# Kernel optimization log

Hardware: AMD Instinct MI355X
Metric: run time of the kernel (lower is better)

Reference implementation:

```python
import jax, jax.numpy as jnp
import numpy as np

B, S, D, H, FF = 2, 2048, 1024, 16, 4096
HD = D // H
EPS = 1e-9


def setup_inputs() -> dict:
    key = jax.random.key(0)
    ks = jax.random.split(key, 16)
    sc = 0.02
    inp = {
        "x": jax.random.normal(ks[0], (B, S, D), jnp.float32),
        "y": jax.random.normal(ks[1], (B, S, D), jnp.float32),
        "decoder_mask": jnp.tril(jnp.ones((S, S), jnp.int32))[None, None],  # [1,1,S,S]
        # self-attention params (weights stored [in,out])
        "qkv_w": jax.random.normal(ks[2], (D, 3 * D), jnp.float32) * sc,
        "qkv_b": jnp.zeros((3 * D,), jnp.float32),
        "sa_fc_w": jax.random.normal(ks[3], (D, D), jnp.float32) * sc,
        "sa_fc_b": jnp.zeros((D,), jnp.float32),
        "g1": jnp.ones((D,), jnp.float32),
        "b1": jnp.zeros((D,), jnp.float32),
        # cross-attention params
        "kv_w": jax.random.normal(ks[4], (D, 2 * D), jnp.float32) * sc,
        "kv_b": jnp.zeros((2 * D,), jnp.float32),
        "q_w": jax.random.normal(ks[5], (D, D), jnp.float32) * sc,
        "q_b": jnp.zeros((D,), jnp.float32),
        "ca_fc_w": jax.random.normal(ks[6], (D, D), jnp.float32) * sc,
        "ca_fc_b": jnp.zeros((D,), jnp.float32),
        "g2": jnp.ones((D,), jnp.float32),
        "b2": jnp.zeros((D,), jnp.float32),
        # FFN params
        "ff1_w": jax.random.normal(ks[7], (D, FF), jnp.float32) * sc,
        "ff1_b": jnp.zeros((FF,), jnp.float32),
        "ff2_w": jax.random.normal(ks[8], (FF, D), jnp.float32) * sc,
        "ff2_b": jnp.zeros((D,), jnp.float32),
        "g3": jnp.ones((D,), jnp.float32),
        "b3": jnp.zeros((D,), jnp.float32),
    }
    return inp


def _layernorm(x, g, b):
    mean = jnp.mean(x, axis=-1, keepdims=True)
    var = jnp.mean((x - mean) ** 2, axis=-1, keepdims=True)
    return g * (x - mean) / jnp.sqrt(var + EPS) + b


def _sdpa(q, k, v, mask=None):
    # q,k,v: [B,H,S,hd]
    scores = jnp.einsum("bhqd,bhkd->bhqk", q, k) / jnp.sqrt(jnp.float32(q.shape[-1]))
    if mask is not None:
        scores = jnp.where(mask == 0, jnp.float32(-1e9), scores)
    attn = jax.nn.softmax(scores, axis=-1)
    return jnp.einsum("bhqk,bhkd->bhqd", attn, v)


def reference(x, y, decoder_mask, qkv_w, qkv_b, sa_fc_w, sa_fc_b, g1, b1,
              kv_w, kv_b, q_w, q_b, ca_fc_w, ca_fc_b, g2, b2,
              ff1_w, ff1_b, ff2_w, ff2_b, g3, b3):
    b, s, d = y.shape
    # --- masked self-attention on y ---
    qkv = (y @ qkv_w + qkv_b).reshape(b, s, H, 3 * HD).transpose(0, 2, 1, 3)
    q, k, v = jnp.split(qkv, 3, axis=-1)
    vals = _sdpa(q, k, v, decoder_mask).transpose(0, 2, 1, 3).reshape(b, s, d)
    sa = vals @ sa_fc_w + sa_fc_b
    y = _layernorm(sa + y, g1, b1)
    # --- cross-attention: kv from x, q from y ---
    kv = (x @ kv_w + kv_b).reshape(b, s, H, 2 * HD).transpose(0, 2, 1, 3)
    k2, v2 = jnp.split(kv, 2, axis=-1)
    q2 = (y @ q_w + q_b).reshape(b, s, H, HD).transpose(0, 2, 1, 3)
    vals2 = _sdpa(q2, k2, v2, None).transpose(0, 2, 1, 3).reshape(b, s, d)
    ca = vals2 @ ca_fc_w + ca_fc_b
    y = _layernorm(ca + y, g2, b2)
    # --- FFN ---
    h = jax.nn.relu(y @ ff1_w + ff1_b)
    ff = h @ ff2_w + ff2_b
    y = _layernorm(ff + y, g3, b3)
    return y
```

## Files before the change

kernel.cpp:

```cpp
#include <hip/hip_runtime.h>

typedef unsigned short u16;
typedef unsigned int u32;
typedef __attribute__((ext_vector_type(4))) float f32x4;
typedef __attribute__((ext_vector_type(8))) __bf16 bf16x8;
typedef __attribute__((ext_vector_type(2))) __bf16 bf16x2;
typedef __attribute__((ext_vector_type(4))) u16 u16x4;

#define NB 2
#define NS 2048
#define ND 1024
#define NH 16
#define NHD 64
#define NFF 4096
#define NBS (NB * NS)

typedef const __attribute__((address_space(1))) unsigned int as1_u32;
typedef __attribute__((address_space(3))) unsigned int as3_u32;

__device__ __forceinline__ void gl_lds16(const u16* g, u16* l) {
  __builtin_amdgcn_global_load_lds((as1_u32*)g, (as3_u32*)l, 16, 0, 0);
}

__device__ __forceinline__ u16 f2bf(float f) {
  union { float f; unsigned u; } v; v.f = f;
  unsigned r = (v.u + 0x7FFFu + ((v.u >> 16) & 1u)) >> 16;
  return (u16)r;
}

__device__ __forceinline__ float bf2f(u16 u) {
  union { u32 u; float f; } v; v.u = ((u32)u) << 16; return v.f;
}

__device__ __forceinline__ u32 pkbf(float a, float b) {
  bf16x2 v; v[0] = (__bf16)a; v[1] = (__bf16)b;
  union { bf16x2 v; u32 u; } c; c.v = v; return c.u;
}

__device__ __forceinline__ char* lswz(void* base, int row, int bcol) {
  return (char*)base + row * 128 + (bcol ^ ((row & 7) << 4));
}
__device__ __forceinline__ const char* lswz(const void* base, int row, int bcol) {
  return (const char*)base + row * 128 + (bcol ^ ((row & 7) << 4));
}

__global__ __launch_bounds__(256) void conv_bf16(const float* __restrict__ in,
                                                 u16* __restrict__ out, int n4) {
  int i = blockIdx.x * 256 + threadIdx.x;
  if (i >= n4) return;
  f32x4 v = *reinterpret_cast<const f32x4*>(&in[(size_t)i * 4]);
  u16x4 o;
#pragma unroll
  for (int j = 0; j < 4; ++j) o[j] = f2bf(v[j]);
  *reinterpret_cast<u16x4*>(&out[(size_t)i * 4]) = o;
}

struct WSeg { const float* src; u16* dst; int N; int tile0; };
struct WAll { WSeg s[7]; };

__global__ void wconv_all(WAll wa) {
  __shared__ float t[32][33];
  int bid = blockIdx.x;
  int si = 0;
#pragma unroll
  for (int i = 1; i < 7; ++i) si += (bid >= wa.s[i].tile0) ? 1 : 0;
  const WSeg sg = wa.s[si];
  const int tt = bid - sg.tile0;
  const int tilesx = sg.N >> 5;
  const int n0 = (tt % tilesx) * 32, k0 = (tt / tilesx) * 32;
  const int K = (si == 6) ? NFF : ND;
  int tx = threadIdx.x, ty = threadIdx.y;
#pragma unroll
  for (int i = ty; i < 32; i += 8) t[i][tx] = sg.src[(size_t)(k0 + i) * sg.N + n0 + tx];
  __syncthreads();
#pragma unroll
  for (int i = ty; i < 32; i += 8)
    sg.dst[(size_t)(n0 + i) * K + k0 + tx] = f2bf(t[tx][i]);
}

template <int TM, int OUTF32, int RELU>
__global__ __launch_bounds__(256) void gemm_bt(const u16* __restrict__ A,
                                               const u16* __restrict__ BT,
                                               const float* __restrict__ bias,
                                               float* __restrict__ Cf,
                                               u16* __restrict__ Cb,
                                               int M, int N, int K) {
  constexpr int MR = TM / 32;
  constexpr int ACH = TM / 64;
  __shared__ __align__(16) u16 lA[2][TM * 32];
  __shared__ __align__(16) u16 lB[2][128 * 32];
  const int tid = threadIdx.x;
  const int lane = tid & 63, wave = tid >> 6;
  const int bm = blockIdx.y * TM, bn = blockIdx.x * 128;
  const int wr = (wave >> 1) * (MR * 16), wc = (wave & 1) * 64;
  const int r16 = lane & 15, kg = lane >> 4;

  f32x4 acc[MR][4] = {};

  auto stage = [&](int buf, int k0) {
#pragma unroll
    for (int c = 0; c < ACH; ++c) {
      int chunk = c * 256 + tid;
      int r = chunk >> 2, kc = (chunk & 3) * 8;
      gl_lds16(&A[(size_t)(bm + r) * K + k0 + kc], &lA[buf][(c * 256 + wave * 64) * 8]);
    }
#pragma unroll
    for (int c = 0; c < 2; ++c) {
      int chunk = c * 256 + tid;
      int r = chunk >> 2, kc = (chunk & 3) * 8;
      gl_lds16(&BT[(size_t)(bn + r) * K + k0 + kc], &lB[buf][(c * 256 + wave * 64) * 8]);
    }
  };

  stage(0, 0);
  __syncthreads();

  const int nk = K / 32;
  for (int i = 0; i < nk; ++i) {
    const int cur = i & 1;
    if (i + 1 < nk) stage(cur ^ 1, (i + 1) * 32);

    bf16x8 af[MR], bfr[4];
#pragma unroll
    for (int m = 0; m < MR; ++m)
      af[m] = *reinterpret_cast<const bf16x8*>(&lA[cur][(wr + m * 16 + r16) * 32 + kg * 8]);
#pragma unroll
    for (int n = 0; n < 4; ++n)
      bfr[n] = *reinterpret_cast<const bf16x8*>(&lB[cur][(wc + n * 16 + r16) * 32 + kg * 8]);
#pragma unroll
    for (int m = 0; m < MR; ++m)
#pragma unroll
      for (int n = 0; n < 4; ++n)
        acc[m][n] = __builtin_amdgcn_mfma_f32_16x16x32_bf16(af[m], bfr[n], acc[m][n], 0, 0, 0);

    __syncthreads();
  }

#pragma unroll
  for (int m = 0; m < MR; ++m) {
    int row = bm + wr + m * 16 + kg * 4;
#pragma unroll
    for (int n = 0; n < 4; ++n) {
      int col = bn + wc + n * 16 + r16;
      float bv = bias[col];
#pragma unroll
      for (int j = 0; j < 4; ++j) {
        float v = acc[m][n][j] + bv;
        if (RELU) v = fmaxf(v, 0.f);
        if (OUTF32)
          Cf[(size_t)(row + j) * N + col] = v;
        else
          Cb[(size_t)(row + j) * N + col] = f2bf(v);
      }
    }
  }
}

__global__ __launch_bounds__(256) void vt_kern(const u16* __restrict__ src, int stride,
                                               int hmul, int hadd, u16* __restrict__ VT) {
  __shared__ u16 lt[64][72];
  const int bh = blockIdx.y;
  const int b = bh >> 4, h = bh & 15;
  const int s0 = blockIdx.x * 64;
  const u16* sb = src + (size_t)b * NS * stride + h * hmul + hadd;
#pragma unroll
  for (int c = 0; c < 2; ++c) {
    int chunk = c * 256 + threadIdx.x;
    int r = chunk >> 3, d = (chunk & 7) * 8;
    *reinterpret_cast<uint4*>(&lt[r][d]) =
        *reinterpret_cast<const uint4*>(&sb[(size_t)(s0 + r) * stride + d]);
  }
  __syncthreads();
  const int d = threadIdx.x >> 2, sq = (threadIdx.x & 3) * 16;
  union { u16 e[16]; uint4 v[2]; } pk;
#pragma unroll
  for (int i = 0; i < 16; ++i) pk.e[i] = lt[sq + i][d];
  uint4* dst = reinterpret_cast<uint4*>(&VT[((size_t)bh * NHD + d) * NS + s0 + sq]);
  dst[0] = pk.v[0];
  dst[1] = pk.v[1];
}

#define C1F 0.180336880f
#define OPSZ ((size_t)32 * NS * NHD)

template <int CAUSAL>
__global__ __launch_bounds__(512) void attn10(const u16* __restrict__ Qp, int qstride,
                                              int qhm, const u16* __restrict__ Kp,
                                              int kstride, int khm, int kha,
                                              const u16* __restrict__ VT,
                                              u16* __restrict__ OP,
                                              float2* __restrict__ ML) {
  const int bid = blockIdx.x;
  const int split = blockIdx.y;
  const int xcd = bid & 7, j5 = bid >> 3;
  const int bh = xcd + 8 * (j5 >> 3);
  int qt = j5 & 7;
  if (CAUSAL) qt = 7 - qt;
  const int b = bh >> 4, h = bh & 15;
  const int tid = threadIdx.x, lane = tid & 63, wave = tid >> 6;
  const int r16 = lane & 15, kg = lane >> 4;
  const int q0w = qt * 256 + wave * 32;

  __shared__ __align__(16) char lK[2][64 * 128];
  __shared__ __align__(16) char lV[2][64 * 128];
  __shared__ __align__(16) char lP[8][16 * 128];
  char* lPw = &lP[wave][0];

  const u16* qb = Qp + (size_t)b * NS * qstride + h * qhm;
  const u16* kb = Kp + (size_t)b * NS * kstride + h * khm + kha;
  const u16* vb = VT + (size_t)bh * NHD * NS;

  const int srow = tid >> 3;
  const int sbcol = (tid & 7) * 16;
  const int scol = (tid & 7) * 8;

  bf16x8 qf[2][2];
#pragma unroll
  for (int qn = 0; qn < 2; ++qn)
#pragma unroll
    for (int ks = 0; ks < 2; ++ks) {
      bf16x8 v = *reinterpret_cast<const bf16x8*>(
          &qb[(size_t)(q0w + qn * 16 + r16) * qstride + ks * 32 + kg * 8]);
#pragma unroll
      for (int e = 0; e < 8; ++e) v[e] = (__bf16)((float)v[e] * C1F);
      qf[qn][ks] = v;
    }

  f32x4 o_acc[2][4] = {};
  float m_run[2] = {-1e30f, -1e30f}, l_lane[2] = {0.f, 0.f};

  const int ntb = CAUSAL ? (4 * qt + 4) : (NS / 64);
  const int wnt = CAUSAL ? (q0w / 64 + 1) : (NS / 64);
  const int halfb = (ntb + 1) >> 1;
  const int t0 = split ? halfb : 0;
  const int t1 = split ? ntb : halfb;

  uint4 kreg, vreg;
  auto ldregs = [&](int t) {
    const int kv0 = t * 64;
    kreg = *reinterpret_cast<const uint4*>(&kb[(size_t)(kv0 + srow) * kstride + scol]);
    vreg = *reinterpret_cast<const uint4*>(&vb[(size_t)srow * NS + kv0 + scol]);
  };
  auto wrlds = [&](int buf) {
    *reinterpret_cast<uint4*>(lswz(lK[buf], srow, sbcol)) = kreg;
    *reinterpret_cast<uint4*>(lswz(lV[buf], srow, sbcol)) = vreg;
  };

  ldregs(t0);
  wrlds(0);
  __syncthreads();

  for (int t = t0; t < t1; ++t) {
    const int cur = (t - t0) & 1;
    const bool more = (t + 1 < t1);
    if (more) ldregs(t + 1);

    if (t < wnt) {
      const int kv0 = t * 64;
      const char* lKc = lK[cur];
      const char* lVc = lV[cur];

      bf16x8 kf[8];
#pragma unroll
      for (int c = 0; c < 4; ++c)
#pragma unroll
        for (int ks = 0; ks < 2; ++ks)
          kf[c * 2 + ks] = *reinterpret_cast<const bf16x8*>(
              lswz(lKc, c * 16 + r16, ks * 64 + kg * 16));

      f32x4 s[2][4] = {};
#pragma unroll
      for (int c = 0; c < 4; ++c)
#pragma unroll
        for (int ks = 0; ks < 2; ++ks) {
          s[0][c] = __builtin_amdgcn_mfma_f32_16x16x32_bf16(kf[c * 2 + ks], qf[0][ks], s[0][c], 0, 0, 0);
          s[1][c] = __builtin_amdgcn_mfma_f32_16x16x32_bf16(kf[c * 2 + ks], qf[1][ks], s[1][c], 0, 0, 0);
        }

      bf16x8 vf[8];
#pragma unroll
      for (int cd = 0; cd < 4; ++cd)
#pragma unroll
        for (int ks = 0; ks < 2; ++ks)
          vf[cd * 2 + ks] = *reinterpret_cast<const bf16x8*>(
              lswz(lVc, cd * 16 + r16, ks * 64 + kg * 16));

#pragma unroll
      for (int qn = 0; qn < 2; ++qn) {
        if (CAUSAL && t == wnt - 1) {
          const int q = q0w + qn * 16 + r16;
#pragma unroll
          for (int c = 0; c < 4; ++c)
#pragma unroll
            for (int j = 0; j < 4; ++j)
              if (kv0 + c * 16 + kg * 4 + j > q) s[qn][c][j] = -1e31f;
        }
        float m0 = fmaxf(fmaxf(s[qn][0][0], s[qn][0][1]), fmaxf(s[qn][0][2], s[qn][0][3]));
        float m1 = fmaxf(fmaxf(s[qn][1][0], s[qn][1][1]), fmaxf(s[qn][1][2], s[qn][1][3]));
        float m2 = fmaxf(fmaxf(s[qn][2][0], s[qn][2][1]), fmaxf(s[qn][2][2], s[qn][2][3]));
        float m3 = fmaxf(fmaxf(s[qn][3][0], s[qn][3][1]), fmaxf(s[qn][3][2], s[qn][3][3]));
        float mxr = fmaxf(fmaxf(m0, m1), fmaxf(m2, m3));
        float mn = m_run[qn];
        if (!__all(mxr <= mn + 8.f)) {
          float mz = mxr;
          mz = fmaxf(mz, __shfl_xor(mz, 16));
          mz = fmaxf(mz, __shfl_xor(mz, 32));
          mn = fmaxf(m_run[qn], mz);
          const float cr = exp2f(m_run[qn] - mn);
          m_run[qn] = mn;
          l_lane[qn] *= cr;
          float crow[4];
#pragma unroll
          for (int j = 0; j < 4; ++j) crow[j] = __shfl(cr, kg * 4 + j);
#pragma unroll
          for (int cd = 0; cd < 4; ++cd)
#pragma unroll
            for (int j = 0; j < 4; ++j) o_acc[qn][cd][j] *= crow[j];
        }
        float su = 0.f;
#pragma unroll
        for (int c = 0; c < 4; ++c)
#pragma unroll
          for (int j = 0; j < 4; ++j) {
            float p = exp2f(s[qn][c][j] - mn);
            s[qn][c][j] = p;
            su += p;
          }
        l_lane[qn] += su;

#pragma unroll
        for (int c = 0; c < 4; ++c) {
          uint2 w2 = {pkbf(s[qn][c][0], s[qn][c][1]), pkbf(s[qn][c][2], s[qn][c][3])};
          *reinterpret_cast<uint2*>(lswz(lPw, r16, c * 32 + kg * 8)) = w2;
        }
        bf16x8 pf[2];
#pragma unroll
        for (int ks = 0; ks < 2; ++ks)
          pf[ks] = *reinterpret_cast<const bf16x8*>(
              lswz(lPw, r16, ks * 64 + kg * 16));
#pragma unroll
        for (int cd = 0; cd < 4; ++cd)
#pragma unroll
          for (int ks = 0; ks < 2; ++ks)
            o_acc[qn][cd] = __builtin_amdgcn_mfma_f32_16x16x32_bf16(
                pf[ks], vf[cd * 2 + ks], o_acc[qn][cd], 0, 0, 0);
      }
    }

    if (more) wrlds(cur ^ 1);
    __syncthreads();
  }

  u16* op = OP + split * OPSZ + (size_t)bh * NS * NHD;
#pragma unroll
  for (int qn = 0; qn < 2; ++qn) {
    float l = l_lane[qn];
    l += __shfl_xor(l, 16);
    l += __shfl_xor(l, 32);
#pragma unroll
    for (int cd = 0; cd < 4; ++cd) {
      int col = cd * 16 + r16;
#pragma unroll
      for (int j = 0; j < 4; ++j) {
        int row = q0w + qn * 16 + kg * 4 + j;
        op[(size_t)row * NHD + col] = f2bf(o_acc[qn][cd][j]);
      }
    }
    if (kg == 0)
      ML[(size_t)split * 32 * NS + (size_t)bh * NS + q0w + qn * 16 + r16] =
          make_float2(m_run[qn], l);
  }
}

__global__ __launch_bounds__(256) void attn_comb(const u16* __restrict__ OP,
                                                 const float2* __restrict__ ML,
                                                 u16* __restrict__ AO) {
  int idx = blockIdx.x * 256 + threadIdx.x;
  int dg = (idx & 7) * 8;
  int q = (idx >> 3) & (NS - 1);
  int bh = idx >> 14;
  int b = bh >> 4, h = bh & 15;
  float2 ml0 = ML[(size_t)bh * NS + q];
  float2 ml1 = ML[(size_t)32 * NS + (size_t)bh * NS + q];
  float M = fmaxf(ml0.x, ml1.x);
  float w0 = exp2f(ml0.x - M), w1 = exp2f(ml1.x - M);
  float linv = 1.f / (ml0.y * w0 + ml1.y * w1);
  w0 *= linv;
  w1 *= linv;
  size_t src = ((size_t)bh * NS + q) * NHD + dg;
  uint4 r0 = *reinterpret_cast<const uint4*>(&OP[src]);
  uint4 r1 = *reinterpret_cast<const uint4*>(&OP[OPSZ + src]);
  const u16* e0 = reinterpret_cast<const u16*>(&r0);
  const u16* e1 = reinterpret_cast<const u16*>(&r1);
  u16 out[8];
#pragma unroll
  for (int j = 0; j < 8; ++j)
    out[j] = f2bf(bf2f(e0[j]) * w0 + bf2f(e1[j]) * w1);
  *reinterpret_cast<uint4*>(&AO[((size_t)b * NS + q) * ND + h * NHD + dg]) =
      *reinterpret_cast<uint4*>(out);
}

__global__ __launch_bounds__(256) void ln_kern(const float* __restrict__ a,
                                               const float* __restrict__ resid,
                                               const float* __restrict__ g,
                                               const float* __restrict__ bb,
                                               float* __restrict__ outf,
                                               u16* __restrict__ outb) {
  const int row = blockIdx.x;
  const int tid = threadIdx.x;
  const size_t off = (size_t)row * ND + tid * 4;
  f32x4 v = *reinterpret_cast<const f32x4*>(&a[off]);
  f32x4 r = *reinterpret_cast<const f32x4*>(&resid[off]);
#pragma unroll
  for (int j = 0; j < 4; ++j) v[j] += r[j];
  float s = v[0] + v[1] + v[2] + v[3];
  float s2 = v[0] * v[0] + v[1] * v[1] + v[2] * v[2] + v[3] * v[3];
#pragma unroll
  for (int m = 1; m < 64; m <<= 1) {
    s += __shfl_xor(s, m);
    s2 += __shfl_xor(s2, m);
  }
  __shared__ float ws1[4], ws2[4];
  int wave = tid >> 6, lane = tid & 63;
  if (lane == 0) { ws1[wave] = s; ws2[wave] = s2; }
  __syncthreads();
  s = ws1[0] + ws1[1] + ws1[2] + ws1[3];
  s2 = ws2[0] + ws2[1] + ws2[2] + ws2[3];
  float mean = s * (1.f / ND);
  float var = fmaxf(s2 * (1.f / ND) - mean * mean, 0.f);
  float rstd = rsqrtf(var + 1e-9f);
  f32x4 gg = *reinterpret_cast<const f32x4*>(&g[tid * 4]);
  f32x4 bv = *reinterpret_cast<const f32x4*>(&bb[tid * 4]);
  f32x4 o;
  u16x4 ob;
#pragma unroll
  for (int j = 0; j < 4; ++j) {
    o[j] = gg[j] * (v[j] - mean) * rstd + bv[j];
    ob[j] = f2bf(o[j]);
  }
  *reinterpret_cast<f32x4*>(&outf[off]) = o;
  *reinterpret_cast<u16x4*>(&outb[off]) = ob;
}

extern "C" void kernel_launch(void* const* d_in, const int* in_sizes, int n_in,
                              void* d_out, int out_size, void* d_ws, size_t ws_size,
                              hipStream_t stream) {
  const float* x = (const float*)d_in[0];
  const float* y = (const float*)d_in[1];
  const float* qkv_w = (const float*)d_in[3];
  const float* qkv_b = (const float*)d_in[4];
  const float* sa_fc_w = (const float*)d_in[5];
  const float* sa_fc_b = (const float*)d_in[6];
  const float* g1 = (const float*)d_in[7];
  const float* b1 = (const float*)d_in[8];
  const float* kv_w = (const float*)d_in[9];
  const float* kv_b = (const float*)d_in[10];
  const float* q_w = (const float*)d_in[11];
  const float* q_b = (const float*)d_in[12];
  const float* ca_fc_w = (const float*)d_in[13];
  const float* ca_fc_b = (const float*)d_in[14];
  const float* g2 = (const float*)d_in[15];
  const float* b2 = (const float*)d_in[16];
  const float* ff1_w = (const float*)d_in[17];
  const float* ff1_b = (const float*)d_in[18];
  const float* ff2_w = (const float*)d_in[19];
  const float* ff2_b = (const float*)d_in[20];
  const float* g3 = (const float*)d_in[21];
  const float* b3 = (const float*)d_in[22];

  if (ws_size < (120ull << 20)) return;

  char* w = (char*)d_ws;
  u16* Wqkv = (u16*)w;
  u16* Wsa  = Wqkv + 3145728;
  u16* Wkv  = Wsa + 1048576;
  u16* Wq   = Wkv + 2097152;
  u16* Wca  = Wq + 1048576;
  u16* Wff1 = Wca + 1048576;
  u16* Wff2 = Wff1 + 4194304;
  u16* ACT = (u16*)(w + (32ull << 20));
  u16* XB  = (u16*)(w + (40ull << 20));
  u16* Qb  = (u16*)(w + (48ull << 20));
  u16* VT  = (u16*)(w + (56ull << 20));
  u16* G   = (u16*)(w + (64ull << 20));
  float* Fa = (float*)(w + (88ull << 20));
  float* Fb = (float*)(w + (104ull << 20));
  u16* H   = XB;
  u16* AO  = G;
  u16* OPb = (u16*)Fa;
  float2* ML = (float2*)ACT;
  float* OUT = (float*)d_out;

  dim3 wblk(32, 8);
  const int n4act = NBS * ND / 4;

  conv_bf16<<<n4act / 256, 256, 0, stream>>>(y, ACT, n4act);
  conv_bf16<<<n4act / 256, 256, 0, stream>>>(x, XB, n4act);
  WAll wa;
  wa.s[0] = {qkv_w, Wqkv, 3 * ND, 0};
  wa.s[1] = {sa_fc_w, Wsa, ND, 3072};
  wa.s[2] = {kv_w, Wkv, 2 * ND, 4096};
  wa.s[3] = {q_w, Wq, ND, 6144};
  wa.s[4] = {ca_fc_w, Wca, ND, 7168};
  wa.s[5] = {ff1_w, Wff1, NFF, 8192};
  wa.s[6] = {ff2_w, Wff2, ND, 12288};
  wconv_all<<<16384, wblk, 0, stream>>>(wa);

  gemm_bt<128, 0, 0><<<dim3(3 * ND / 128, NBS / 128), 256, 0, stream>>>(
      ACT, Wqkv, qkv_b, nullptr, G, NBS, 3 * ND, ND);
  vt_kern<<<dim3(NS / 64, NB * NH), 256, 0, stream>>>(G, 3 * ND, 192, 128, VT);
  attn10<1><<<dim3(256, 2), 512, 0, stream>>>(G, 3 * ND, 192, G, 3 * ND, 192, 64, VT, OPb, ML);
  attn_comb<<<2048, 256, 0, stream>>>(OPb, ML, AO);
  gemm_bt<64, 1, 0><<<dim3(ND / 128, NBS / 64), 256, 0, stream>>>(
      AO, Wsa, sa_fc_b, Fa, nullptr, NBS, ND, ND);
  ln_kern<<<NBS, 256, 0, stream>>>(Fa, y, g1, b1, Fb, ACT);

  gemm_bt<128, 0, 0><<<dim3(2 * ND / 128, NBS / 128), 256, 0, stream>>>(
      XB, Wkv, kv_b, nullptr, G, NBS, 2 * ND, ND);
  vt_kern<<<dim3(NS / 64, NB * NH), 256, 0, stream>>>(G, 2 * ND, 128, 64, VT);
  gemm_bt<64, 0, 0><<<dim3(ND / 128, NBS / 64), 256, 0, stream>>>(
      ACT, Wq, q_b, nullptr, Qb, NBS, ND, ND);
  attn10<0><<<dim3(256, 2), 512, 0, stream>>>(Qb, ND, 64, G, 2 * ND, 128, 0, VT, OPb, ML);
  attn_comb<<<2048, 256, 0, stream>>>(OPb, ML, AO);
  gemm_bt<64, 1, 0><<<dim3(ND / 128, NBS / 64), 256, 0, stream>>>(
      AO, Wca, ca_fc_b, Fa, nullptr, NBS, ND, ND);
  ln_kern<<<NBS, 256, 0, stream>>>(Fa, Fb, g2, b2, Fb, ACT);

  gemm_bt<128, 0, 1><<<dim3(NFF / 128, NBS / 128), 256, 0, stream>>>(
      ACT, Wff1, ff1_b, nullptr, H, NBS, NFF, ND);
  gemm_bt<64, 1, 0><<<dim3(ND / 128, NBS / 64), 256, 0, stream>>>(
      H, Wff2, ff2_b, Fa, nullptr, NBS, ND, NFF);
  ln_kern<<<NBS, 256, 0, stream>>>(Fa, Fb, g3, b3, OUT, ACT);
}
```

Before: 465.9 us.

## Split causal attention four ways, sum softmax rows via MFMA, swizzle GEMM blocks

Causal self-attention now splits each query tile's key range into four chunks instead of two, so more workgroups share the long causal tiles. A generalized combine kernel merges any number of partial results. The softmax row sum is now an MFMA against a vector of ones, replacing the scalar adds and cross-lane shuffles. GEMM workgroup indices are remapped in strides of eight, likely to group tiles per XCD for cache reuse, and MFMA sections are wrapped in s_setprio. The risk is extra partial-output traffic and combine work, and the output and ML buffers must be large enough for four splits.

```diff
diff --git a/kernel.cpp b/kernel.cpp
--- a/kernel.cpp
+++ b/kernel.cpp
@@ -91,7 +91,11 @@
   __shared__ __align__(16) u16 lB[2][128 * 32];
   const int tid = threadIdx.x;
   const int lane = tid & 63, wave = tid >> 6;
-  const int bm = blockIdx.y * TM, bn = blockIdx.x * 128;
+  const u32 gx = gridDim.x;
+  const u32 nwg = gx * gridDim.y;
+  const u32 flat = blockIdx.y * gx + blockIdx.x;
+  const u32 swz = (flat & 7) * (nwg >> 3) + (flat >> 3);
+  const int bm = (swz / gx) * TM, bn = (swz % gx) * 128;
   const int wr = (wave >> 1) * (MR * 16), wc = (wave & 1) * 64;
   const int r16 = lane & 15, kg = lane >> 4;
 
@@ -127,11 +131,13 @@
 #pragma unroll
     for (int n = 0; n < 4; ++n)
       bfr[n] = *reinterpret_cast<const bf16x8*>(&lB[cur][(wc + n * 16 + r16) * 32 + kg * 8]);
+    __builtin_amdgcn_s_setprio(1);
 #pragma unroll
     for (int m = 0; m < MR; ++m)
 #pragma unroll
       for (int n = 0; n < 4; ++n)
         acc[m][n] = __builtin_amdgcn_mfma_f32_16x16x32_bf16(af[m], bfr[n], acc[m][n], 0, 0, 0);
+    __builtin_amdgcn_s_setprio(0);
 
     __syncthreads();
   }
@@ -183,8 +189,8 @@
 #define C1F 0.180336880f
 #define OPSZ ((size_t)32 * NS * NHD)
 
-template <int CAUSAL>
-__global__ __launch_bounds__(512) void attn10(const u16* __restrict__ Qp, int qstride,
+template <int CAUSAL, int SPLITS>
+__global__ __launch_bounds__(512) void attn11(const u16* __restrict__ Qp, int qstride,
                                               int qhm, const u16* __restrict__ Kp,
                                               int kstride, int khm, int kha,
                                               const u16* __restrict__ VT,
@@ -226,14 +232,18 @@
       qf[qn][ks] = v;
     }
 
+  bf16x8 onesf;
+#pragma unroll
+  for (int e = 0; e < 8; ++e) onesf[e] = (__bf16)1.0f;
+
   f32x4 o_acc[2][4] = {};
-  float m_run[2] = {-1e30f, -1e30f}, l_lane[2] = {0.f, 0.f};
+  f32x4 l_acc[2] = {};
+  float m_run[2] = {-1e30f, -1e30f};
 
   const int ntb = CAUSAL ? (4 * qt + 4) : (NS / 64);
   const int wnt = CAUSAL ? (q0w / 64 + 1) : (NS / 64);
-  const int halfb = (ntb + 1) >> 1;
-  const int t0 = split ? halfb : 0;
-  const int t1 = split ? ntb : halfb;
+  const int t0 = (split * ntb) / SPLITS;
+  const int t1 = ((split + 1) * ntb) / SPLITS;
 
   uint4 kreg, vreg;
   auto ldregs = [&](int t) {
@@ -269,6 +279,7 @@
               lswz(lKc, c * 16 + r16, ks * 64 + kg * 16));
 
       f32x4 s[2][4] = {};
+      __builtin_amdgcn_s_setprio(1);
 #pragma unroll
       for (int c = 0; c < 4; ++c)
 #pragma unroll
@@ -276,6 +287,7 @@
           s[0][c] = __builtin_amdgcn_mfma_f32_16x16x32_bf16(kf[c * 2 + ks], qf[0][ks], s[0][c], 0, 0, 0);
           s[1][c] = __builtin_amdgcn_mfma_f32_16x16x32_bf16(kf[c * 2 + ks], qf[1][ks], s[1][c], 0, 0, 0);
         }
+      __builtin_amdgcn_s_setprio(0);
 
       bf16x8 vf[8];
 #pragma unroll
@@ -308,7 +320,6 @@
           mn = fmaxf(m_run[qn], mz);
           const float cr = exp2f(m_run[qn] - mn);
           m_run[qn] = mn;
-          l_lane[qn] *= cr;
           float crow[4];
 #pragma unroll
           for (int j = 0; j < 4; ++j) crow[j] = __shfl(cr, kg * 4 + j);
@@ -316,17 +327,14 @@
           for (int cd = 0; cd < 4; ++cd)
 #pragma unroll
             for (int j = 0; j < 4; ++j) o_acc[qn][cd][j] *= crow[j];
+#pragma unroll
+          for (int j = 0; j < 4; ++j) l_acc[qn][j] *= crow[j];
         }
-        float su = 0.f;
 #pragma unroll
         for (int c = 0; c < 4; ++c)
 #pragma unroll
-          for (int j = 0; j < 4; ++j) {
-            float p = exp2f(s[qn][c][j] - mn);
-            s[qn][c][j] = p;
-            su += p;
-          }
-        l_lane[qn] += su;
+          for (int j = 0; j < 4; ++j)
+            s[qn][c][j] = exp2f(s[qn][c][j] - mn);
 
 #pragma unroll
         for (int c = 0; c < 4; ++c) {
@@ -336,14 +344,18 @@
         bf16x8 pf[2];
 #pragma unroll
         for (int ks = 0; ks < 2; ++ks)
-          pf[ks] = *reinterpret_cast<const bf16x8*>(
-              lswz(lPw, r16, ks * 64 + kg * 16));
+          pf[ks] = *reinterpret_cast<const bf16x8*>(lswz(lPw, r16, ks * 64 + kg * 16));
+
+        __builtin_amdgcn_s_setprio(1);
+        l_acc[qn] = __builtin_amdgcn_mfma_f32_16x16x32_bf16(pf[0], onesf, l_acc[qn], 0, 0, 0);
+        l_acc[qn] = __builtin_amdgcn_mfma_f32_16x16x32_bf16(pf[1], onesf, l_acc[qn], 0, 0, 0);
 #pragma unroll
         for (int cd = 0; cd < 4; ++cd)
 #pragma unroll
           for (int ks = 0; ks < 2; ++ks)
             o_acc[qn][cd] = __builtin_amdgcn_mfma_f32_16x16x32_bf16(
                 pf[ks], vf[cd * 2 + ks], o_acc[qn][cd], 0, 0, 0);
+        __builtin_amdgcn_s_setprio(0);
       }
     }
 
@@ -354,9 +366,9 @@
   u16* op = OP + split * OPSZ + (size_t)bh * NS * NHD;
 #pragma unroll
   for (int qn = 0; qn < 2; ++qn) {
-    float l = l_lane[qn];
-    l += __shfl_xor(l, 16);
-    l += __shfl_xor(l, 32);
+    float mrow[4];
+#pragma unroll
+    for (int j = 0; j < 4; ++j) mrow[j] = __shfl(m_run[qn], kg * 4 + j);
 #pragma unroll
     for (int cd = 0; cd < 4; ++cd) {
       int col = cd * 16 + r16;
@@ -366,12 +378,16 @@
         op[(size_t)row * NHD + col] = f2bf(o_acc[qn][cd][j]);
       }
     }
-    if (kg == 0)
-      ML[(size_t)split * 32 * NS + (size_t)bh * NS + q0w + qn * 16 + r16] =
-          make_float2(m_run[qn], l);
-  }
-}
-
+    if (r16 == 0) {
+#pragma unroll
+      for (int j = 0; j < 4; ++j)
+        ML[((size_t)(split * 32 + bh)) * NS + q0w + qn * 16 + kg * 4 + j] =
+            make_float2(mrow[j], l_acc[qn][j]);
+    }
+  }
+}
+
+template <int NSPL>
 __global__ __launch_bounds__(256) void attn_comb(const u16* __restrict__ OP,
                                                  const float2* __restrict__ ML,
                                                  u16* __restrict__ AO) {
@@ -380,22 +396,32 @@
   int q = (idx >> 3) & (NS - 1);
   int bh = idx >> 14;
   int b = bh >> 4, h = bh & 15;
-  float2 ml0 = ML[(size_t)bh * NS + q];
-  float2 ml1 = ML[(size_t)32 * NS + (size_t)bh * NS + q];
-  float M = fmaxf(ml0.x, ml1.x);
-  float w0 = exp2f(ml0.x - M), w1 = exp2f(ml1.x - M);
-  float linv = 1.f / (ml0.y * w0 + ml1.y * w1);
-  w0 *= linv;
-  w1 *= linv;
+  float2 ml[NSPL];
+  float M = -1e30f;
+#pragma unroll
+  for (int s = 0; s < NSPL; ++s) {
+    ml[s] = ML[((size_t)(s * 32 + bh)) * NS + q];
+    M = fmaxf(M, ml[s].x);
+  }
+  float wgt[NSPL], wsum = 0.f;
+#pragma unroll
+  for (int s = 0; s < NSPL; ++s) {
+    wgt[s] = exp2f(ml[s].x - M);
+    wsum += ml[s].y * wgt[s];
+  }
+  float linv = 1.f / wsum;
   size_t src = ((size_t)bh * NS + q) * NHD + dg;
-  uint4 r0 = *reinterpret_cast<const uint4*>(&OP[src]);
-  uint4 r1 = *reinterpret_cast<const uint4*>(&OP[OPSZ + src]);
-  const u16* e0 = reinterpret_cast<const u16*>(&r0);
-  const u16* e1 = reinterpret_cast<const u16*>(&r1);
+  float acc[8] = {};
+#pragma unroll
+  for (int s = 0; s < NSPL; ++s) {
+    uint4 r = *reinterpret_cast<const uint4*>(&OP[s * OPSZ + src]);
+    const u16* e = reinterpret_cast<const u16*>(&r);
+#pragma unroll
+    for (int j = 0; j < 8; ++j) acc[j] += bf2f(e[j]) * wgt[s];
+  }
   u16 out[8];
 #pragma unroll
-  for (int j = 0; j < 8; ++j)
-    out[j] = f2bf(bf2f(e0[j]) * w0 + bf2f(e1[j]) * w1);
+  for (int j = 0; j < 8; ++j) out[j] = f2bf(acc[j] * linv);
   *reinterpret_cast<uint4*>(&AO[((size_t)b * NS + q) * ND + h * NHD + dg]) =
       *reinterpret_cast<uint4*>(out);
 }
@@ -509,8 +535,8 @@
   gemm_bt<128, 0, 0><<<dim3(3 * ND / 128, NBS / 128), 256, 0, stream>>>(
       ACT, Wqkv, qkv_b, nullptr, G, NBS, 3 * ND, ND);
   vt_kern<<<dim3(NS / 64, NB * NH), 256, 0, stream>>>(G, 3 * ND, 192, 128, VT);
-  attn10<1><<<dim3(256, 2), 512, 0, stream>>>(G, 3 * ND, 192, G, 3 * ND, 192, 64, VT, OPb, ML);
-  attn_comb<<<2048, 256, 0, stream>>>(OPb, ML, AO);
+  attn11<1, 4><<<dim3(256, 4), 512, 0, stream>>>(G, 3 * ND, 192, G, 3 * ND, 192, 64, VT, OPb, ML);
+  attn_comb<4><<<2048, 256, 0, stream>>>(OPb, ML, AO);
   gemm_bt<64, 1, 0><<<dim3(ND / 128, NBS / 64), 256, 0, stream>>>(
       AO, Wsa, sa_fc_b, Fa, nullptr, NBS, ND, ND);
   ln_kern<<<NBS, 256, 0, stream>>>(Fa, y, g1, b1, Fb, ACT);
@@ -520,8 +546,8 @@
   vt_kern<<<dim3(NS / 64, NB * NH), 256, 0, stream>>>(G, 2 * ND, 128, 64, VT);
   gemm_bt<64, 0, 0><<<dim3(ND / 128, NBS / 64), 256, 0, stream>>>(
       ACT, Wq, q_b, nullptr, Qb, NBS, ND, ND);
-  attn10<0><<<dim3(256, 2), 512, 0, stream>>>(Qb, ND, 64, G, 2 * ND, 128, 0, VT, OPb, ML);
-  attn_comb<<<2048, 256, 0, stream>>>(OPb, ML, AO);
+  attn11<0, 2><<<dim3(256, 2), 512, 0, stream>>>(Qb, ND, 64, G, 2 * ND, 128, 0, VT, OPb, ML);
+  attn_comb<2><<<2048, 256, 0, stream>>>(OPb, ML, AO);
   gemm_bt<64, 1, 0><<<dim3(ND / 128, NBS / 64), 256, 0, stream>>>(
       AO, Wca, ca_fc_b, Fa, nullptr, NBS, ND, ND);
   ln_kern<<<NBS, 256, 0, stream>>>(Fa, Fb, g2, b2, Fb, ACT);
```

After: 462.6 us. Within noise of the previous version (-0.7%).
